# Optimization experiments

Measured on AMD Instinct MI355X. Metric: run time of the kernel, lower is better.

Reference implementation:

```python
import jax, jax.numpy as jnp
import numpy as np

# dims mirroring the torch module: dim=32 (MVN), omega=8, d_head=n_embd//n_head
B, T, E, DH = 8, 2048, 1024, 32
OMEGA, DIM = 8, 32
M = OMEGA * DIM  # 256 random features (omega concatenated N(0, I_dim) samples)


def setup_inputs() -> dict:
    key = jax.random.key(0)
    ks = jax.random.split(key, 8)
    s = 1.0 / np.sqrt(E).astype(np.float32)  # torch Linear-like init scale
    return {
        "x": jax.random.normal(ks[0], (B, T, E), jnp.float32),
        "Wq": jax.random.normal(ks[1], (E, DH), jnp.float32) * s,
        "bq": jax.random.normal(ks[2], (DH,), jnp.float32) * s,
        "Wk": jax.random.normal(ks[3], (E, DH), jnp.float32) * s,
        "bk": jax.random.normal(ks[4], (DH,), jnp.float32) * s,
        "Wv": jax.random.normal(ks[5], (E, DH), jnp.float32) * s,
        "bv": jax.random.normal(ks[6], (DH,), jnp.float32) * s,
        # random-feature matrix: omega stacked samples from N(0, I_DIM) -> [M, DH]
        "w": jax.random.normal(ks[7], (M, DH), jnp.float32),
    }


def reference(x, Wq, bq, Wk, bk, Wv, bv, w):
    # projections (as in Head.forward)
    q = x @ Wq + bq  # [B,T,DH]
    k = x @ Wk + bk  # [B,T,DH]
    v = x @ Wv + bv  # computed but unused, exactly as in the source
    del v
    # Aprox_softmax (FAVOR+-style hyperbolic random features), vectorized per token
    z = k + q                                          # [B,T,DH]
    zsqr = jnp.sum(k * k, -1) + jnp.sum(q * q, -1)     # [B,T]  (per-token norms)
    A = jnp.exp(-0.5 * zsqr)                           # [B,T]
    cosH = jnp.cosh(jnp.einsum('btd,md->btm', z, w))   # [B,T,M]
    R = A[..., None] * cosH                            # [B,T,M]
    return R
```

## Files before the change

### kernel.cpp

```cpp
#include <hip/hip_runtime.h>
#include <cstdint>

#define E_DIM   1024
#define DH      32
#define M_FEAT  256
#define BT      16384

typedef __attribute__((ext_vector_type(8))) _Float16 f16x8;
typedef __attribute__((ext_vector_type(4))) float f32x4;


__device__ __forceinline__ unsigned packh2(_Float16 a, _Float16 b) {
    union { _Float16 h[2]; unsigned u; } t;
    t.h[0] = a; t.h[1] = b;
    return t.u;
}

__device__ __forceinline__ void splitf16_2(float f0, float f1, unsigned& ph, unsigned& pl) {
    _Float16 h0 = (_Float16)f0, h1 = (_Float16)f1;
    float l0 = f0 - (float)h0, l1 = f1 - (float)h1;
    ph = packh2(h0, h1);
    pl = packh2((_Float16)l0, (_Float16)l1);
}

__device__ __forceinline__ void splitf16_8(const float4& a, const float4& b,
                                           uint4& uh, uint4& ul) {
    splitf16_2(a.x, a.y, uh.x, ul.x);
    splitf16_2(a.z, a.w, uh.y, ul.y);
    splitf16_2(b.x, b.y, uh.z, ul.z);
    splitf16_2(b.z, b.w, uh.w, ul.w);
}

__global__ __launch_bounds__(256) void k_prep(
    const float* __restrict__ Wq, const float* __restrict__ Wk,
    short* __restrict__ ws)
{
    __shared__ float wlds[64 * 36];
    const int b = blockIdx.x, tid = threadIdx.x;
    const float* __restrict__ src = (b < 16) ? Wq : Wk;
    const int k0 = (b & 15) * 64;
    const int nbase = (b < 16) ? 0 : 32;
#pragma unroll
    for (int it = 0; it < 2; ++it) {
        int f = it * 256 + tid;
        int k = f >> 3, c4 = f & 7;
        float4 v = *(const float4*)(src + (size_t)(k0 + k) * DH + c4 * 4);
        *(float4*)&wlds[k * 36 + c4 * 4] = v;
    }
    __syncthreads();
    const int n = tid >> 3, kq = tid & 7;
    const int n_g = nbase + n;
    const int nt = n_g >> 4, ln = n_g & 15;
#pragma unroll
    for (int rep = 0; rep < 2; ++rep) {
        int kk = rep * 8 + kq;
        int k_g = k0 + kk * 4;
        float f0 = wlds[(kk * 4 + 0) * 36 + n];
        float f1 = wlds[(kk * 4 + 1) * 36 + n];
        float f2 = wlds[(kk * 4 + 2) * 36 + n];
        float f3 = wlds[(kk * 4 + 3) * 36 + n];
        uint2 ph;
        ph.x = packh2((_Float16)f0, (_Float16)f1);
        ph.y = packh2((_Float16)f2, (_Float16)f3);
        int sub = k_g >> 5;
        int gq = (k_g >> 3) & 3, j0 = k_g & 7;
        int lane = gq * 16 + ln;
        size_t flat = ((size_t)(nt * 32 + sub)) * 512 + lane * 8 + j0;
        *(uint2*)(ws + flat) = ph;
    }
}

#define TB 32
#define XS2 136
#define QS 68
#define ZS 40

__global__ __launch_bounds__(256, 3) void k_main(
    const float* __restrict__ x, const float* __restrict__ bq,
    const float* __restrict__ bk, const short* __restrict__ ws,
    const float* __restrict__ w, float* __restrict__ out)
{
    __shared__ __align__(16) short xh_s[2][TB * XS2];
    __shared__ __align__(16) short xl_s[2][TB * XS2];
    __shared__ __align__(16) float qk_f[TB * QS];
    __shared__ __align__(16) short zh_s[TB * ZS];
    __shared__ __align__(16) short zl_s[TB * ZS];
    __shared__ float lnA_f[TB];

    const int tid  = threadIdx.x;
    const int lane = tid & 63;
    const int wv   = __builtin_amdgcn_readfirstlane(tid >> 6);
    const int ln15 = lane & 15;
    const int g    = lane >> 4;
    const long t0  = (long)blockIdx.x * TB;

    const int nrow = wv * 16 + ln15;
    const float bias = (nrow < 32) ? bq[nrow] : bk[nrow - 32];

    const int kq = tid & 15;
    const int mr = tid >> 4;

    f32x4 acc0 = {0.f, 0.f, 0.f, 0.f};
    f32x4 acc1 = {0.f, 0.f, 0.f, 0.f};

    const short* wpB = ws + (size_t)(wv * 32) * 512 + lane * 8;
    const float* xr0 = x + (t0 + mr) * (size_t)E_DIM + kq * 8;
    const float* xr1 = x + (t0 + mr + 16) * (size_t)E_DIM + kq * 8;

    float4 a0 = *(const float4*)(xr0 + 0), b0 = *(const float4*)(xr0 + 4);
    float4 a1 = *(const float4*)(xr1 + 0), b1 = *(const float4*)(xr1 + 4);
    {
        uint4 uh, ul;
        splitf16_8(a0, b0, uh, ul);
        *(uint4*)&xh_s[0][mr * XS2 + kq * 8] = uh;
        *(uint4*)&xl_s[0][mr * XS2 + kq * 8] = ul;
        splitf16_8(a1, b1, uh, ul);
        *(uint4*)&xh_s[0][(mr + 16) * XS2 + kq * 8] = uh;
        *(uint4*)&xl_s[0][(mr + 16) * XS2 + kq * 8] = ul;
    }

#pragma unroll
    for (int p = 0; p < 8; ++p) {
        __syncthreads();
        if (p < 7) {
            a0 = *(const float4*)(xr0 + (p + 1) * 128);
            b0 = *(const float4*)(xr0 + (p + 1) * 128 + 4);
            a1 = *(const float4*)(xr1 + (p + 1) * 128);
            b1 = *(const float4*)(xr1 + (p + 1) * 128 + 4);
        }
#pragma unroll
        for (int j = 0; j < 4; ++j) {
            f16x8 bh = *(const f16x8*)(wpB + (size_t)(p * 4 + j) * 512);
            f16x8 ah0 = *(const f16x8*)&xh_s[p & 1][ln15 * XS2 + j * 32 + g * 8];
            f16x8 al0 = *(const f16x8*)&xl_s[p & 1][ln15 * XS2 + j * 32 + g * 8];
            f16x8 ah1 = *(const f16x8*)&xh_s[p & 1][(ln15 + 16) * XS2 + j * 32 + g * 8];
            f16x8 al1 = *(const f16x8*)&xl_s[p & 1][(ln15 + 16) * XS2 + j * 32 + g * 8];
            acc0 = __builtin_amdgcn_mfma_f32_16x16x32_f16(ah0, bh, acc0, 0, 0, 0);
            acc0 = __builtin_amdgcn_mfma_f32_16x16x32_f16(al0, bh, acc0, 0, 0, 0);
            acc1 = __builtin_amdgcn_mfma_f32_16x16x32_f16(ah1, bh, acc1, 0, 0, 0);
            acc1 = __builtin_amdgcn_mfma_f32_16x16x32_f16(al1, bh, acc1, 0, 0, 0);
        }
        if (p < 7) {
            uint4 uh, ul;
            splitf16_8(a0, b0, uh, ul);
            *(uint4*)&xh_s[(p + 1) & 1][mr * XS2 + kq * 8] = uh;
            *(uint4*)&xl_s[(p + 1) & 1][mr * XS2 + kq * 8] = ul;
            splitf16_8(a1, b1, uh, ul);
            *(uint4*)&xh_s[(p + 1) & 1][(mr + 16) * XS2 + kq * 8] = uh;
            *(uint4*)&xl_s[(p + 1) & 1][(mr + 16) * XS2 + kq * 8] = ul;
        }
    }

    float4 wfa[4], wfb[4];
#pragma unroll
    for (int i = 0; i < 4; ++i) {
        const int nf = (wv * 4 + i) * 16 + ln15;
        wfa[i] = *(const float4*)(w + (size_t)nf * DH + g * 8);
        wfb[i] = *(const float4*)(w + (size_t)nf * DH + g * 8 + 4);
    }

#pragma unroll
    for (int r = 0; r < 4; ++r) {
        qk_f[(g * 4 + r) * QS + nrow]        = acc0[r] + bias;
        qk_f[(16 + g * 4 + r) * QS + nrow]   = acc1[r] + bias;
    }
    __syncthreads();

    {
        const int tok = tid >> 3, grp = tid & 7;
        float4 qv = *(const float4*)&qk_f[tok * QS + grp * 4];
        float4 kv = *(const float4*)&qk_f[tok * QS + 32 + grp * 4];
        float z0 = qv.x + kv.x, z1 = qv.y + kv.y, z2 = qv.z + kv.z, z3 = qv.w + kv.w;
        float pw = qv.x*qv.x + qv.y*qv.y + qv.z*qv.z + qv.w*qv.w
                 + kv.x*kv.x + kv.y*kv.y + kv.z*kv.z + kv.w*kv.w;
        uint2 ph, pl;
        splitf16_2(z0, z1, ph.x, pl.x);
        splitf16_2(z2, z3, ph.y, pl.y);
        *(uint2*)&zh_s[tok * ZS + grp * 4] = ph;
        *(uint2*)&zl_s[tok * ZS + grp * 4] = pl;
        pw += __shfl_xor(pw, 1);
        pw += __shfl_xor(pw, 2);
        pw += __shfl_xor(pw, 4);
        if (grp == 0) lnA_f[tok] = -0.5f * pw;
    }
    __syncthreads();

    f32x4 facc[4][2];
#pragma unroll
    for (int i = 0; i < 4; ++i)
#pragma unroll
        for (int mt = 0; mt < 2; ++mt) facc[i][mt] = (f32x4){0.f,0.f,0.f,0.f};

    f16x8 a_h[2], a_l[2];
#pragma unroll
    for (int mt = 0; mt < 2; ++mt) {
        a_h[mt] = *(const f16x8*)&zh_s[(mt * 16 + ln15) * ZS + g * 8];
        a_l[mt] = *(const f16x8*)&zl_s[(mt * 16 + ln15) * ZS + g * 8];
    }
#pragma unroll
    for (int i = 0; i < 4; ++i) {
        uint4 uw;
        uw.x = packh2((_Float16)wfa[i].x, (_Float16)wfa[i].y);
        uw.y = packh2((_Float16)wfa[i].z, (_Float16)wfa[i].w);
        uw.z = packh2((_Float16)wfb[i].x, (_Float16)wfb[i].y);
        uw.w = packh2((_Float16)wfb[i].z, (_Float16)wfb[i].w);
        f16x8 w8 = __builtin_bit_cast(f16x8, uw);
#pragma unroll
        for (int mt = 0; mt < 2; ++mt) {
            facc[i][mt] = __builtin_amdgcn_mfma_f32_16x16x32_f16(a_h[mt], w8, facc[i][mt], 0, 0, 0);
            facc[i][mt] = __builtin_amdgcn_mfma_f32_16x16x32_f16(a_l[mt], w8, facc[i][mt], 0, 0, 0);
        }
    }

    float lnAv[2][4];
#pragma unroll
    for (int mt = 0; mt < 2; ++mt)
#pragma unroll
        for (int r = 0; r < 4; ++r) lnAv[mt][r] = lnA_f[mt * 16 + g * 4 + r];

#pragma unroll
    for (int i = 0; i < 4; ++i) {
        const int n = (wv * 4 + i) * 16 + ln15;
#pragma unroll
        for (int mt = 0; mt < 2; ++mt) {
#pragma unroll
            for (int r = 0; r < 4; ++r) {
                float s = facc[i][mt][r];
                float R = 0.5f * (__expf(lnAv[mt][r] + s) + __expf(lnAv[mt][r] - s));
                __builtin_nontemporal_store(R, &out[(t0 + mt * 16 + g * 4 + r) * M_FEAT + n]);
            }
        }
    }
}

extern "C" void kernel_launch(void* const* d_in, const int* in_sizes, int n_in,
                              void* d_out, int out_size, void* d_ws, size_t ws_size,
                              hipStream_t stream) {
    const float* x  = (const float*)d_in[0];
    const float* Wq = (const float*)d_in[1];
    const float* bq = (const float*)d_in[2];
    const float* Wk = (const float*)d_in[3];
    const float* bk = (const float*)d_in[4];
    const float* w  = (const float*)d_in[7];
    float* out = (float*)d_out;
    short* ws  = (short*)d_ws;

    k_prep<<<dim3(32), dim3(256), 0, stream>>>(Wq, Wk, ws);
    k_main<<<dim3(BT / TB), dim3(256), 0, stream>>>(x, bq, bk, ws, w, out);
}
```

Before: 120.9 us.

## Use single-wave blocks of 16 tokens with register-pipelined weight loads

Restructures the main kernel from 256-thread blocks of 32 tokens into 64-thread single-wave blocks of 16 tokens. Each wave now computes all 64 q/k projection columns itself and prefetches the packed weight fragments into registers with a three-deep ring. Because q/k, z and the norm stay within one wave, the block-wide barriers go away and the norm reduction is done with shuffles. The random-feature weights are also double-buffered in registers. In exchange the fp16-packed weights are read from global memory once per 16 tokens instead of once per 32, which doubles that traffic, and register pressure per wave goes up.

```diff
diff --git a/kernel.cpp b/kernel.cpp
--- a/kernel.cpp
+++ b/kernel.cpp
@@ -70,164 +70,172 @@
     }
 }
 
-#define TB 32
 #define XS2 136
-#define QS 68
-#define ZS 40
-
-__global__ __launch_bounds__(256, 3) void k_main(
+#define ZSF 36
+
+__global__ __launch_bounds__(64, 2) void k_main(
     const float* __restrict__ x, const float* __restrict__ bq,
     const float* __restrict__ bk, const short* __restrict__ ws,
     const float* __restrict__ w, float* __restrict__ out)
 {
-    __shared__ __align__(16) short xh_s[2][TB * XS2];
-    __shared__ __align__(16) short xl_s[2][TB * XS2];
-    __shared__ __align__(16) float qk_f[TB * QS];
-    __shared__ __align__(16) short zh_s[TB * ZS];
-    __shared__ __align__(16) short zl_s[TB * ZS];
-    __shared__ float lnA_f[TB];
-
-    const int tid  = threadIdx.x;
-    const int lane = tid & 63;
-    const int wv   = __builtin_amdgcn_readfirstlane(tid >> 6);
+    __shared__ __align__(16) short xh_s[2][16 * XS2];
+    __shared__ __align__(16) short xl_s[2][16 * XS2];
+    __shared__ __align__(16) float zf_s[16 * ZSF];
+
+    const int lane = threadIdx.x;
     const int ln15 = lane & 15;
     const int g    = lane >> 4;
-    const long t0  = (long)blockIdx.x * TB;
-
-    const int nrow = wv * 16 + ln15;
-    const float bias = (nrow < 32) ? bq[nrow] : bk[nrow - 32];
-
-    const int kq = tid & 15;
-    const int mr = tid >> 4;
-
-    f32x4 acc0 = {0.f, 0.f, 0.f, 0.f};
-    f32x4 acc1 = {0.f, 0.f, 0.f, 0.f};
-
-    const short* wpB = ws + (size_t)(wv * 32) * 512 + lane * 8;
-    const float* xr0 = x + (t0 + mr) * (size_t)E_DIM + kq * 8;
-    const float* xr1 = x + (t0 + mr + 16) * (size_t)E_DIM + kq * 8;
-
-    float4 a0 = *(const float4*)(xr0 + 0), b0 = *(const float4*)(xr0 + 4);
-    float4 a1 = *(const float4*)(xr1 + 0), b1 = *(const float4*)(xr1 + 4);
+    const long t0  = (long)blockIdx.x * 16;
+
+    f32x4 acc[4];
+#pragma unroll
+    for (int nt = 0; nt < 4; ++nt) acc[nt] = (f32x4){0.f, 0.f, 0.f, 0.f};
+
+    const short* wpB = ws + lane * 8;
+
+    const float* xrow0 = x + (t0 + 0 * 4 + g) * (size_t)E_DIM + ln15 * 8;
+    const float* xrow1 = x + (t0 + 1 * 4 + g) * (size_t)E_DIM + ln15 * 8;
+    const float* xrow2 = x + (t0 + 2 * 4 + g) * (size_t)E_DIM + ln15 * 8;
+    const float* xrow3 = x + (t0 + 3 * 4 + g) * (size_t)E_DIM + ln15 * 8;
+
+    float4 xb[8];
+    f16x8 bg[3][4];
+
+    xb[0] = *(const float4*)(xrow0 + 0); xb[1] = *(const float4*)(xrow0 + 4);
+    xb[2] = *(const float4*)(xrow1 + 0); xb[3] = *(const float4*)(xrow1 + 4);
+    xb[4] = *(const float4*)(xrow2 + 0); xb[5] = *(const float4*)(xrow2 + 4);
+    xb[6] = *(const float4*)(xrow3 + 0); xb[7] = *(const float4*)(xrow3 + 4);
+#pragma unroll
+    for (int nt = 0; nt < 4; ++nt)
+        bg[0][nt] = *(const f16x8*)(wpB + ((size_t)nt * 32 + 0) * 512);
+#pragma unroll
+    for (int nt = 0; nt < 4; ++nt)
+        bg[1][nt] = *(const f16x8*)(wpB + ((size_t)nt * 32 + 1) * 512);
     {
         uint4 uh, ul;
-        splitf16_8(a0, b0, uh, ul);
-        *(uint4*)&xh_s[0][mr * XS2 + kq * 8] = uh;
-        *(uint4*)&xl_s[0][mr * XS2 + kq * 8] = ul;
-        splitf16_8(a1, b1, uh, ul);
-        *(uint4*)&xh_s[0][(mr + 16) * XS2 + kq * 8] = uh;
-        *(uint4*)&xl_s[0][(mr + 16) * XS2 + kq * 8] = ul;
-    }
+        splitf16_8(xb[0], xb[1], uh, ul);
+        *(uint4*)&xh_s[0][(0 * 4 + g) * XS2 + ln15 * 8] = uh;
+        *(uint4*)&xl_s[0][(0 * 4 + g) * XS2 + ln15 * 8] = ul;
+        splitf16_8(xb[2], xb[3], uh, ul);
+        *(uint4*)&xh_s[0][(1 * 4 + g) * XS2 + ln15 * 8] = uh;
+        *(uint4*)&xl_s[0][(1 * 4 + g) * XS2 + ln15 * 8] = ul;
+        splitf16_8(xb[4], xb[5], uh, ul);
+        *(uint4*)&xh_s[0][(2 * 4 + g) * XS2 + ln15 * 8] = uh;
+        *(uint4*)&xl_s[0][(2 * 4 + g) * XS2 + ln15 * 8] = ul;
+        splitf16_8(xb[6], xb[7], uh, ul);
+        *(uint4*)&xh_s[0][(3 * 4 + g) * XS2 + ln15 * 8] = uh;
+        *(uint4*)&xl_s[0][(3 * 4 + g) * XS2 + ln15 * 8] = ul;
+    }
+    xb[0] = *(const float4*)(xrow0 + 128); xb[1] = *(const float4*)(xrow0 + 132);
+    xb[2] = *(const float4*)(xrow1 + 128); xb[3] = *(const float4*)(xrow1 + 132);
+    xb[4] = *(const float4*)(xrow2 + 128); xb[5] = *(const float4*)(xrow2 + 132);
+    xb[6] = *(const float4*)(xrow3 + 128); xb[7] = *(const float4*)(xrow3 + 132);
 
 #pragma unroll
     for (int p = 0; p < 8; ++p) {
-        __syncthreads();
-        if (p < 7) {
-            a0 = *(const float4*)(xr0 + (p + 1) * 128);
-            b0 = *(const float4*)(xr0 + (p + 1) * 128 + 4);
-            a1 = *(const float4*)(xr1 + (p + 1) * 128);
-            b1 = *(const float4*)(xr1 + (p + 1) * 128 + 4);
-        }
 #pragma unroll
         for (int j = 0; j < 4; ++j) {
-            f16x8 bh = *(const f16x8*)(wpB + (size_t)(p * 4 + j) * 512);
-            f16x8 ah0 = *(const f16x8*)&xh_s[p & 1][ln15 * XS2 + j * 32 + g * 8];
-            f16x8 al0 = *(const f16x8*)&xl_s[p & 1][ln15 * XS2 + j * 32 + g * 8];
-            f16x8 ah1 = *(const f16x8*)&xh_s[p & 1][(ln15 + 16) * XS2 + j * 32 + g * 8];
-            f16x8 al1 = *(const f16x8*)&xl_s[p & 1][(ln15 + 16) * XS2 + j * 32 + g * 8];
-            acc0 = __builtin_amdgcn_mfma_f32_16x16x32_f16(ah0, bh, acc0, 0, 0, 0);
-            acc0 = __builtin_amdgcn_mfma_f32_16x16x32_f16(al0, bh, acc0, 0, 0, 0);
-            acc1 = __builtin_amdgcn_mfma_f32_16x16x32_f16(ah1, bh, acc1, 0, 0, 0);
-            acc1 = __builtin_amdgcn_mfma_f32_16x16x32_f16(al1, bh, acc1, 0, 0, 0);
+            const int fi = p * 4 + j;
+            if (fi + 2 < 32) {
+#pragma unroll
+                for (int nt = 0; nt < 4; ++nt)
+                    bg[(fi + 2) % 3][nt] =
+                        *(const f16x8*)(wpB + ((size_t)nt * 32 + fi + 2) * 512);
+            }
+            f16x8 ah = *(const f16x8*)&xh_s[p & 1][ln15 * XS2 + j * 32 + g * 8];
+            f16x8 al = *(const f16x8*)&xl_s[p & 1][ln15 * XS2 + j * 32 + g * 8];
+#pragma unroll
+            for (int nt = 0; nt < 4; ++nt)
+                acc[nt] = __builtin_amdgcn_mfma_f32_16x16x32_f16(ah, bg[fi % 3][nt], acc[nt], 0, 0, 0);
+#pragma unroll
+            for (int nt = 0; nt < 4; ++nt)
+                acc[nt] = __builtin_amdgcn_mfma_f32_16x16x32_f16(al, bg[fi % 3][nt], acc[nt], 0, 0, 0);
         }
         if (p < 7) {
             uint4 uh, ul;
-            splitf16_8(a0, b0, uh, ul);
-            *(uint4*)&xh_s[(p + 1) & 1][mr * XS2 + kq * 8] = uh;
-            *(uint4*)&xl_s[(p + 1) & 1][mr * XS2 + kq * 8] = ul;
-            splitf16_8(a1, b1, uh, ul);
-            *(uint4*)&xh_s[(p + 1) & 1][(mr + 16) * XS2 + kq * 8] = uh;
-            *(uint4*)&xl_s[(p + 1) & 1][(mr + 16) * XS2 + kq * 8] = ul;
-        }
-    }
-
-    float4 wfa[4], wfb[4];
-#pragma unroll
-    for (int i = 0; i < 4; ++i) {
-        const int nf = (wv * 4 + i) * 16 + ln15;
-        wfa[i] = *(const float4*)(w + (size_t)nf * DH + g * 8);
-        wfb[i] = *(const float4*)(w + (size_t)nf * DH + g * 8 + 4);
-    }
-
+            splitf16_8(xb[0], xb[1], uh, ul);
+            *(uint4*)&xh_s[(p + 1) & 1][(0 * 4 + g) * XS2 + ln15 * 8] = uh;
+            *(uint4*)&xl_s[(p + 1) & 1][(0 * 4 + g) * XS2 + ln15 * 8] = ul;
+            splitf16_8(xb[2], xb[3], uh, ul);
+            *(uint4*)&xh_s[(p + 1) & 1][(1 * 4 + g) * XS2 + ln15 * 8] = uh;
+            *(uint4*)&xl_s[(p + 1) & 1][(1 * 4 + g) * XS2 + ln15 * 8] = ul;
+            splitf16_8(xb[4], xb[5], uh, ul);
+            *(uint4*)&xh_s[(p + 1) & 1][(2 * 4 + g) * XS2 + ln15 * 8] = uh;
+            *(uint4*)&xl_s[(p + 1) & 1][(2 * 4 + g) * XS2 + ln15 * 8] = ul;
+            splitf16_8(xb[6], xb[7], uh, ul);
+            *(uint4*)&xh_s[(p + 1) & 1][(3 * 4 + g) * XS2 + ln15 * 8] = uh;
+            *(uint4*)&xl_s[(p + 1) & 1][(3 * 4 + g) * XS2 + ln15 * 8] = ul;
+            if (p < 6) {
+                xb[0] = *(const float4*)(xrow0 + (p + 2) * 128);
+                xb[1] = *(const float4*)(xrow0 + (p + 2) * 128 + 4);
+                xb[2] = *(const float4*)(xrow1 + (p + 2) * 128);
+                xb[3] = *(const float4*)(xrow1 + (p + 2) * 128 + 4);
+                xb[4] = *(const float4*)(xrow2 + (p + 2) * 128);
+                xb[5] = *(const float4*)(xrow2 + (p + 2) * 128 + 4);
+                xb[6] = *(const float4*)(xrow3 + (p + 2) * 128);
+                xb[7] = *(const float4*)(xrow3 + (p + 2) * 128 + 4);
+            }
+        }
+    }
+
+    const float b0 = bq[ln15], b1 = bq[16 + ln15];
+    const float b2 = bk[ln15], b3 = bk[16 + ln15];
+    float lnAv[4];
 #pragma unroll
     for (int r = 0; r < 4; ++r) {
-        qk_f[(g * 4 + r) * QS + nrow]        = acc0[r] + bias;
-        qk_f[(16 + g * 4 + r) * QS + nrow]   = acc1[r] + bias;
-    }
-    __syncthreads();
-
-    {
-        const int tok = tid >> 3, grp = tid & 7;
-        float4 qv = *(const float4*)&qk_f[tok * QS + grp * 4];
-        float4 kv = *(const float4*)&qk_f[tok * QS + 32 + grp * 4];
-        float z0 = qv.x + kv.x, z1 = qv.y + kv.y, z2 = qv.z + kv.z, z3 = qv.w + kv.w;
-        float pw = qv.x*qv.x + qv.y*qv.y + qv.z*qv.z + qv.w*qv.w
-                 + kv.x*kv.x + kv.y*kv.y + kv.z*kv.z + kv.w*kv.w;
-        uint2 ph, pl;
-        splitf16_2(z0, z1, ph.x, pl.x);
-        splitf16_2(z2, z3, ph.y, pl.y);
-        *(uint2*)&zh_s[tok * ZS + grp * 4] = ph;
-        *(uint2*)&zl_s[tok * ZS + grp * 4] = pl;
+        float q0 = acc[0][r] + b0, q1 = acc[1][r] + b1;
+        float k0 = acc[2][r] + b2, k1 = acc[3][r] + b3;
+        zf_s[(g * 4 + r) * ZSF + ln15]      = q0 + k0;
+        zf_s[(g * 4 + r) * ZSF + 16 + ln15] = q1 + k1;
+        float pw = q0 * q0 + q1 * q1 + k0 * k0 + k1 * k1;
         pw += __shfl_xor(pw, 1);
         pw += __shfl_xor(pw, 2);
         pw += __shfl_xor(pw, 4);
-        if (grp == 0) lnA_f[tok] = -0.5f * pw;
-    }
-    __syncthreads();
-
-    f32x4 facc[4][2];
-#pragma unroll
-    for (int i = 0; i < 4; ++i)
-#pragma unroll
-        for (int mt = 0; mt < 2; ++mt) facc[i][mt] = (f32x4){0.f,0.f,0.f,0.f};
-
-    f16x8 a_h[2], a_l[2];
-#pragma unroll
-    for (int mt = 0; mt < 2; ++mt) {
-        a_h[mt] = *(const f16x8*)&zh_s[(mt * 16 + ln15) * ZS + g * 8];
-        a_l[mt] = *(const f16x8*)&zl_s[(mt * 16 + ln15) * ZS + g * 8];
-    }
-#pragma unroll
-    for (int i = 0; i < 4; ++i) {
-        uint4 uw;
-        uw.x = packh2((_Float16)wfa[i].x, (_Float16)wfa[i].y);
-        uw.y = packh2((_Float16)wfa[i].z, (_Float16)wfa[i].w);
-        uw.z = packh2((_Float16)wfb[i].x, (_Float16)wfb[i].y);
-        uw.w = packh2((_Float16)wfb[i].z, (_Float16)wfb[i].w);
-        f16x8 w8 = __builtin_bit_cast(f16x8, uw);
-#pragma unroll
-        for (int mt = 0; mt < 2; ++mt) {
-            facc[i][mt] = __builtin_amdgcn_mfma_f32_16x16x32_f16(a_h[mt], w8, facc[i][mt], 0, 0, 0);
-            facc[i][mt] = __builtin_amdgcn_mfma_f32_16x16x32_f16(a_l[mt], w8, facc[i][mt], 0, 0, 0);
-        }
-    }
-
-    float lnAv[2][4];
-#pragma unroll
-    for (int mt = 0; mt < 2; ++mt)
-#pragma unroll
-        for (int r = 0; r < 4; ++r) lnAv[mt][r] = lnA_f[mt * 16 + g * 4 + r];
-
-#pragma unroll
-    for (int i = 0; i < 4; ++i) {
-        const int n = (wv * 4 + i) * 16 + ln15;
-#pragma unroll
-        for (int mt = 0; mt < 2; ++mt) {
+        pw += __shfl_xor(pw, 8);
+        lnAv[r] = -0.5f * pw;
+    }
+
+    float4 za = *(const float4*)&zf_s[ln15 * ZSF + g * 8];
+    float4 zb = *(const float4*)&zf_s[ln15 * ZSF + g * 8 + 4];
+    uint4 zuh, zul;
+    splitf16_8(za, zb, zuh, zul);
+    f16x8 a_h = __builtin_bit_cast(f16x8, zuh);
+    f16x8 a_l = __builtin_bit_cast(f16x8, zul);
+
+    float4 wf[2][8];
+#pragma unroll
+    for (int t = 0; t < 4; ++t) {
+        const int nf = t * 16 + ln15;
+        wf[0][2 * t]     = *(const float4*)(w + (size_t)nf * DH + g * 8);
+        wf[0][2 * t + 1] = *(const float4*)(w + (size_t)nf * DH + g * 8 + 4);
+    }
+#pragma unroll
+    for (int gi = 0; gi < 4; ++gi) {
+        if (gi < 3) {
+#pragma unroll
+            for (int t = 0; t < 4; ++t) {
+                const int nf = ((gi + 1) * 4 + t) * 16 + ln15;
+                wf[(gi + 1) & 1][2 * t]     = *(const float4*)(w + (size_t)nf * DH + g * 8);
+                wf[(gi + 1) & 1][2 * t + 1] = *(const float4*)(w + (size_t)nf * DH + g * 8 + 4);
+            }
+        }
+#pragma unroll
+        for (int t = 0; t < 4; ++t) {
+            uint4 uw;
+            uw.x = packh2((_Float16)wf[gi & 1][2 * t].x,     (_Float16)wf[gi & 1][2 * t].y);
+            uw.y = packh2((_Float16)wf[gi & 1][2 * t].z,     (_Float16)wf[gi & 1][2 * t].w);
+            uw.z = packh2((_Float16)wf[gi & 1][2 * t + 1].x, (_Float16)wf[gi & 1][2 * t + 1].y);
+            uw.w = packh2((_Float16)wf[gi & 1][2 * t + 1].z, (_Float16)wf[gi & 1][2 * t + 1].w);
+            f16x8 w8 = __builtin_bit_cast(f16x8, uw);
+            f32x4 fa = (f32x4){0.f, 0.f, 0.f, 0.f};
+            fa = __builtin_amdgcn_mfma_f32_16x16x32_f16(a_h, w8, fa, 0, 0, 0);
+            fa = __builtin_amdgcn_mfma_f32_16x16x32_f16(a_l, w8, fa, 0, 0, 0);
+            const int n = (gi * 4 + t) * 16 + ln15;
 #pragma unroll
             for (int r = 0; r < 4; ++r) {
-                float s = facc[i][mt][r];
-                float R = 0.5f * (__expf(lnAv[mt][r] + s) + __expf(lnAv[mt][r] - s));
-                __builtin_nontemporal_store(R, &out[(t0 + mt * 16 + g * 4 + r) * M_FEAT + n]);
+                float s = fa[r];
+                float R = 0.5f * (__expf(lnAv[r] + s) + __expf(lnAv[r] - s));
+                __builtin_nontemporal_store(R, &out[(t0 + g * 4 + r) * M_FEAT + n]);
             }
         }
     }
@@ -246,5 +254,5 @@
     short* ws  = (short*)d_ws;
 
     k_prep<<<dim3(32), dim3(256), 0, stream>>>(Wq, Wk, ws);
-    k_main<<<dim3(BT / TB), dim3(256), 0, stream>>>(x, bq, bk, ws, w, out);
-}
+    k_main<<<dim3(BT / 16), dim3(64), 0, stream>>>(x, bq, bk, ws, w, out);
+}
```

Result: slower. 129.9 us (+7.5%).

## Split projection K-dimension across waves with LDS reduction, 16 tokens per block

Applied to the files above, without the earlier changes.

Each block now handles 16 tokens instead of 32. Each wave computes all 64 q/k outputs over a quarter of the 1024-wide K dimension, loading x directly into registers and converting it to fp16 hi/lo there, with no LDS staging and no per-chunk barriers. The four partial sums are reduced through LDS before the feature stage. This removes the double-buffered LDS pipeline and its syncs and doubles the grid size. The cost is more register pressure from holding all x loads and B fragments in flight, plus an extra LDS reduction.

```diff
diff --git a/kernel.cpp b/kernel.cpp
--- a/kernel.cpp
+++ b/kernel.cpp
@@ -70,8 +70,6 @@
     }
 }
 
-#define TB 32
-#define XS2 136
 #define QS 68
 #define ZS 40
 
@@ -80,76 +78,60 @@
     const float* __restrict__ bk, const short* __restrict__ ws,
     const float* __restrict__ w, float* __restrict__ out)
 {
-    __shared__ __align__(16) short xh_s[2][TB * XS2];
-    __shared__ __align__(16) short xl_s[2][TB * XS2];
-    __shared__ __align__(16) float qk_f[TB * QS];
-    __shared__ __align__(16) short zh_s[TB * ZS];
-    __shared__ __align__(16) short zl_s[TB * ZS];
-    __shared__ float lnA_f[TB];
+    __shared__ __align__(16) float red_s[4][4 * 256];
+    __shared__ __align__(16) float qk_f[16 * QS];
+    __shared__ __align__(16) short zh_s[16 * ZS];
+    __shared__ __align__(16) short zl_s[16 * ZS];
+    __shared__ float lnA_f[16];
 
     const int tid  = threadIdx.x;
     const int lane = tid & 63;
     const int wv   = __builtin_amdgcn_readfirstlane(tid >> 6);
     const int ln15 = lane & 15;
     const int g    = lane >> 4;
-    const long t0  = (long)blockIdx.x * TB;
-
-    const int nrow = wv * 16 + ln15;
-    const float bias = (nrow < 32) ? bq[nrow] : bk[nrow - 32];
-
-    const int kq = tid & 15;
-    const int mr = tid >> 4;
-
-    f32x4 acc0 = {0.f, 0.f, 0.f, 0.f};
-    f32x4 acc1 = {0.f, 0.f, 0.f, 0.f};
-
-    const short* wpB = ws + (size_t)(wv * 32) * 512 + lane * 8;
-    const float* xr0 = x + (t0 + mr) * (size_t)E_DIM + kq * 8;
-    const float* xr1 = x + (t0 + mr + 16) * (size_t)E_DIM + kq * 8;
-
-    float4 a0 = *(const float4*)(xr0 + 0), b0 = *(const float4*)(xr0 + 4);
-    float4 a1 = *(const float4*)(xr1 + 0), b1 = *(const float4*)(xr1 + 4);
-    {
+    const long t0  = (long)blockIdx.x * 16;
+
+    const float* __restrict__ xA = x + (t0 + ln15) * (size_t)E_DIM + wv * 256 + g * 8;
+    float4 a[8][2];
+#pragma unroll
+    for (int fi = 0; fi < 8; ++fi) {
+        a[fi][0] = *(const float4*)(xA + fi * 32);
+        a[fi][1] = *(const float4*)(xA + fi * 32 + 4);
+    }
+    const short* __restrict__ wpB = ws + (size_t)(wv * 8) * 512 + lane * 8;
+    f16x8 bg[3][4];
+#pragma unroll
+    for (int q = 0; q < 3; ++q)
+#pragma unroll
+        for (int nt = 0; nt < 4; ++nt)
+            bg[q][nt] = *(const f16x8*)(wpB + ((size_t)nt * 32 + q) * 512);
+
+    f32x4 acc[4];
+#pragma unroll
+    for (int nt = 0; nt < 4; ++nt) acc[nt] = (f32x4){0.f, 0.f, 0.f, 0.f};
+
+#pragma unroll
+    for (int fi = 0; fi < 8; ++fi) {
         uint4 uh, ul;
-        splitf16_8(a0, b0, uh, ul);
-        *(uint4*)&xh_s[0][mr * XS2 + kq * 8] = uh;
-        *(uint4*)&xl_s[0][mr * XS2 + kq * 8] = ul;
-        splitf16_8(a1, b1, uh, ul);
-        *(uint4*)&xh_s[0][(mr + 16) * XS2 + kq * 8] = uh;
-        *(uint4*)&xl_s[0][(mr + 16) * XS2 + kq * 8] = ul;
-    }
-
-#pragma unroll
-    for (int p = 0; p < 8; ++p) {
-        __syncthreads();
-        if (p < 7) {
-            a0 = *(const float4*)(xr0 + (p + 1) * 128);
-            b0 = *(const float4*)(xr0 + (p + 1) * 128 + 4);
-            a1 = *(const float4*)(xr1 + (p + 1) * 128);
-            b1 = *(const float4*)(xr1 + (p + 1) * 128 + 4);
+        splitf16_8(a[fi][0], a[fi][1], uh, ul);
+        f16x8 ah = __builtin_bit_cast(f16x8, uh);
+        f16x8 al = __builtin_bit_cast(f16x8, ul);
+#pragma unroll
+        for (int nt = 0; nt < 4; ++nt)
+            acc[nt] = __builtin_amdgcn_mfma_f32_16x16x32_f16(ah, bg[fi % 3][nt], acc[nt], 0, 0, 0);
+#pragma unroll
+        for (int nt = 0; nt < 4; ++nt)
+            acc[nt] = __builtin_amdgcn_mfma_f32_16x16x32_f16(al, bg[fi % 3][nt], acc[nt], 0, 0, 0);
+        if (fi + 3 < 8) {
+#pragma unroll
+            for (int nt = 0; nt < 4; ++nt)
+                bg[fi % 3][nt] = *(const f16x8*)(wpB + ((size_t)nt * 32 + fi + 3) * 512);
         }
-#pragma unroll
-        for (int j = 0; j < 4; ++j) {
-            f16x8 bh = *(const f16x8*)(wpB + (size_t)(p * 4 + j) * 512);
-            f16x8 ah0 = *(const f16x8*)&xh_s[p & 1][ln15 * XS2 + j * 32 + g * 8];
-            f16x8 al0 = *(const f16x8*)&xl_s[p & 1][ln15 * XS2 + j * 32 + g * 8];
-            f16x8 ah1 = *(const f16x8*)&xh_s[p & 1][(ln15 + 16) * XS2 + j * 32 + g * 8];
-            f16x8 al1 = *(const f16x8*)&xl_s[p & 1][(ln15 + 16) * XS2 + j * 32 + g * 8];
-            acc0 = __builtin_amdgcn_mfma_f32_16x16x32_f16(ah0, bh, acc0, 0, 0, 0);
-            acc0 = __builtin_amdgcn_mfma_f32_16x16x32_f16(al0, bh, acc0, 0, 0, 0);
-            acc1 = __builtin_amdgcn_mfma_f32_16x16x32_f16(ah1, bh, acc1, 0, 0, 0);
-            acc1 = __builtin_amdgcn_mfma_f32_16x16x32_f16(al1, bh, acc1, 0, 0, 0);
-        }
-        if (p < 7) {
-            uint4 uh, ul;
-            splitf16_8(a0, b0, uh, ul);
-            *(uint4*)&xh_s[(p + 1) & 1][mr * XS2 + kq * 8] = uh;
-            *(uint4*)&xl_s[(p + 1) & 1][mr * XS2 + kq * 8] = ul;
-            splitf16_8(a1, b1, uh, ul);
-            *(uint4*)&xh_s[(p + 1) & 1][(mr + 16) * XS2 + kq * 8] = uh;
-            *(uint4*)&xl_s[(p + 1) & 1][(mr + 16) * XS2 + kq * 8] = ul;
-        }
-    }
+    }
+
+#pragma unroll
+    for (int nt = 0; nt < 4; ++nt)
+        *(f32x4*)&red_s[wv][nt * 256 + g * 64 + ln15 * 4] = acc[nt];
 
     float4 wfa[4], wfb[4];
 #pragma unroll
@@ -158,15 +140,22 @@
         wfa[i] = *(const float4*)(w + (size_t)nf * DH + g * 8);
         wfb[i] = *(const float4*)(w + (size_t)nf * DH + g * 8 + 4);
     }
-
-#pragma unroll
-    for (int r = 0; r < 4; ++r) {
-        qk_f[(g * 4 + r) * QS + nrow]        = acc0[r] + bias;
-        qk_f[(16 + g * 4 + r) * QS + nrow]   = acc1[r] + bias;
-    }
-    __syncthreads();
-
-    {
+    __syncthreads();
+
+    f32x4 c = (f32x4){0.f, 0.f, 0.f, 0.f};
+#pragma unroll
+    for (int w2 = 0; w2 < 4; ++w2) {
+        f32x4 t = *(const f32x4*)&red_s[w2][wv * 256 + g * 64 + ln15 * 4];
+        c[0] += t[0]; c[1] += t[1]; c[2] += t[2]; c[3] += t[3];
+    }
+    const int nrow = wv * 16 + ln15;
+    const float bias = (nrow < 32) ? bq[nrow] : bk[nrow - 32];
+#pragma unroll
+    for (int r = 0; r < 4; ++r)
+        qk_f[(g * 4 + r) * QS + nrow] = c[r] + bias;
+    __syncthreads();
+
+    if (tid < 128) {
         const int tok = tid >> 3, grp = tid & 7;
         float4 qv = *(const float4*)&qk_f[tok * QS + grp * 4];
         float4 kv = *(const float4*)&qk_f[tok * QS + 32 + grp * 4];
@@ -185,18 +174,12 @@
     }
     __syncthreads();
 
-    f32x4 facc[4][2];
-#pragma unroll
-    for (int i = 0; i < 4; ++i)
-#pragma unroll
-        for (int mt = 0; mt < 2; ++mt) facc[i][mt] = (f32x4){0.f,0.f,0.f,0.f};
-
-    f16x8 a_h[2], a_l[2];
-#pragma unroll
-    for (int mt = 0; mt < 2; ++mt) {
-        a_h[mt] = *(const f16x8*)&zh_s[(mt * 16 + ln15) * ZS + g * 8];
-        a_l[mt] = *(const f16x8*)&zl_s[(mt * 16 + ln15) * ZS + g * 8];
-    }
+    f32x4 facc[4];
+#pragma unroll
+    for (int i = 0; i < 4; ++i) facc[i] = (f32x4){0.f, 0.f, 0.f, 0.f};
+
+    f16x8 a_h = *(const f16x8*)&zh_s[ln15 * ZS + g * 8];
+    f16x8 a_l = *(const f16x8*)&zl_s[ln15 * ZS + g * 8];
 #pragma unroll
     for (int i = 0; i < 4; ++i) {
         uint4 uw;
@@ -205,30 +188,22 @@
         uw.z = packh2((_Float16)wfb[i].x, (_Float16)wfb[i].y);
         uw.w = packh2((_Float16)wfb[i].z, (_Float16)wfb[i].w);
         f16x8 w8 = __builtin_bit_cast(f16x8, uw);
-#pragma unroll
-        for (int mt = 0; mt < 2; ++mt) {
-            facc[i][mt] = __builtin_amdgcn_mfma_f32_16x16x32_f16(a_h[mt], w8, facc[i][mt], 0, 0, 0);
-            facc[i][mt] = __builtin_amdgcn_mfma_f32_16x16x32_f16(a_l[mt], w8, facc[i][mt], 0, 0, 0);
-        }
-    }
-
-    float lnAv[2][4];
-#pragma unroll
-    for (int mt = 0; mt < 2; ++mt)
-#pragma unroll
-        for (int r = 0; r < 4; ++r) lnAv[mt][r] = lnA_f[mt * 16 + g * 4 + r];
+        facc[i] = __builtin_amdgcn_mfma_f32_16x16x32_f16(a_h, w8, facc[i], 0, 0, 0);
+        facc[i] = __builtin_amdgcn_mfma_f32_16x16x32_f16(a_l, w8, facc[i], 0, 0, 0);
+    }
+
+    float lnAv[4];
+#pragma unroll
+    for (int r = 0; r < 4; ++r) lnAv[r] = lnA_f[g * 4 + r];
 
 #pragma unroll
     for (int i = 0; i < 4; ++i) {
         const int n = (wv * 4 + i) * 16 + ln15;
 #pragma unroll
-        for (int mt = 0; mt < 2; ++mt) {
-#pragma unroll
-            for (int r = 0; r < 4; ++r) {
-                float s = facc[i][mt][r];
-                float R = 0.5f * (__expf(lnAv[mt][r] + s) + __expf(lnAv[mt][r] - s));
-                __builtin_nontemporal_store(R, &out[(t0 + mt * 16 + g * 4 + r) * M_FEAT + n]);
-            }
+        for (int r = 0; r < 4; ++r) {
+            float s = facc[i][r];
+            float R = 0.5f * (__expf(lnAv[r] + s) + __expf(lnAv[r] - s));
+            __builtin_nontemporal_store(R, &out[(t0 + g * 4 + r) * M_FEAT + n]);
         }
     }
 }
@@ -246,5 +221,5 @@
     short* ws  = (short*)d_ws;
 
     k_prep<<<dim3(32), dim3(256), 0, stream>>>(Wq, Wk, ws);
-    k_main<<<dim3(BT / TB), dim3(256), 0, stream>>>(x, bq, bk, ws, w, out);
-}
+    k_main<<<dim3(BT / 16), dim3(256), 0, stream>>>(x, bq, bk, ws, w, out);
+}
```

After: 126.1 us. 1.04x slower.
